# Kernel tuning notes

Measured on AMD Instinct MI355X. Metric: run time of the kernel, lower is better.

## Reference

```python
import jax, jax.numpy as jnp
import numpy as np

N_COARSE = 262145   # GMGN self.n
K_LEVELS = 5        # self.k
M_NBR = 9           # self.m
HID = 2048          # hidden_channels


def _build_grid():
    # replicates GMGN.init_toep_kernel (mtype='toep_mg')
    n_fine = 2 * (N_COARSE - 1) + 1          # 524289
    x = np.linspace(-1.0, 1.0, n_fine)
    x_lst, idx_lst = [], []
    for _ in range(K_LEVELS):
        n = x.shape[0]
        idx = np.arange((n - 1) // 2 - M_NBR + 1, (n - 1) // 2 + M_NBR)[1::2]  # m-1 center pts
        idx_lst.append(idx)
        x_lst.append(x[idx])
        x = x[::2]                            # injection1d
    x_lst.append(x)                           # coarse grid
    xs = np.concatenate(x_lst)[:, None].astype(np.float32)   # (N_eval, 1)
    nbrs = np.stack(idx_lst[::-1]).astype(np.int64)          # (k, m-1), coarse->fine
    return xs, nbrs


def setup_inputs() -> dict:
    key = jax.random.key(0)
    xs_np, nbrs_np = _build_grid()
    dims = [1, HID, HID, HID, HID, 1]
    inp = {"xs": jnp.asarray(xs_np), "nbrs": jnp.asarray(nbrs_np), "k": K_LEVELS, "m": M_NBR}
    ks = jax.random.split(key, 10)
    for j in range(5):
        bd = 1.0 / np.sqrt(dims[j])           # nn.Linear default init range
        inp[f"w{j}"] = jax.random.uniform(ks[2 * j], (dims[j], dims[j + 1]), jnp.float32, -bd, bd)
        inp[f"b{j}"] = jax.random.uniform(ks[2 * j + 1], (dims[j + 1],), jnp.float32, -bd, bd)
    return inp


def _interp1d(a):
    # linear prolongation: (n,) -> (2n-1,); even slots copy, odd slots average
    out = jnp.zeros((2 * a.shape[0] - 1,), a.dtype)
    out = out.at[0::2].set(a)
    return out.at[1::2].set(0.5 * (a[:-1] + a[1:]))


def _forward(xs, Ws, bs, nbrs, k, m):
    h = xs
    for W, b in zip(Ws, bs):
        h = jax.nn.relu(h @ W + b)            # MLP appends relu after every Linear (incl. last)
    Amg = h[:, 0]                             # (N_eval,) pointwise kernel values
    band = m - 1
    Abands = [Amg[band * i: band * (i + 1)] for i in range(k)][::-1]
    Ah = Amg[band * k:]                       # coarse kernel, length (n0-1)/2^k + 1
    for i in range(k):
        Ah = _interp1d(Ah)                    # upsample one level
        Ah = Ah.at[nbrs[i]].set(Abands[i])    # overwrite center band with exact MLP evals
    return Ah[None, None]                     # (1, 1, 2*(n-1)+1)


def reference(xs, w0, b0, w1, b1, w2, b2, w3, b3, w4, b4, nbrs, k, m):
    return _forward(xs, (w0, w1, w2, w3, w4), (b0, b1, b2, b3, b4), nbrs, k, m)
```

## Files before the change

### kernel.cpp

```cpp
#include <hip/hip_runtime.h>
#include <stdint.h>

#define HID    2048
#define MPTS   16425
#define MTILES 129
#define NTIL   16
#define KTIL   64
#define BIMG   5120

typedef float    f32x4 __attribute__((ext_vector_type(4)));
typedef _Float16 f16x8 __attribute__((ext_vector_type(8)));


__global__ void pack_w16(const float* __restrict__ w1,
                         const float* __restrict__ w2,
                         const float* __restrict__ w3,
                         _Float16* __restrict__ wp) {
    const int kt = blockIdx.x, nt = blockIdx.y, L = blockIdx.z;
    const float* W = (L == 0) ? w1 : ((L == 1) ? w2 : w3);
    __shared__ float tl[128 * 33];
    const int tid = threadIdx.x;
    const int k  = tid >> 3;
    const int nc = (tid & 7) * 16;
    const float* src = W + (size_t)(kt * 32 + k) * HID + nt * 128 + nc;
    #pragma unroll
    for (int j = 0; j < 16; ++j) tl[(nc + j) * 33 + k] = src[j];
    __syncthreads();
    const size_t base = (size_t)(L * 1024 + nt * 64 + kt) * BIMG;
    for (int e = tid; e < BIMG; e += 256) {
        int n = e / 40, kk = e - n * 40;
        wp[base + e] = (kk < 32) ? (_Float16)tl[n * 33 + kk] : (_Float16)0.f;
    }
}

__launch_bounds__(256, 3)
__global__ void gemm_hl(const _Float16* __restrict__ Ahg,
                        const _Float16* __restrict__ Alg,
                        const _Float16* __restrict__ wp,
                        const float* __restrict__ bias,
                        _Float16* __restrict__ Chg,
                        _Float16* __restrict__ Clg,
                        int layer, int write_lo,
                        float* __restrict__ Amg4,
                        const float* __restrict__ w4g, int row0) {
    __shared__ _Float16 Bs[4][BIMG];

    const int tid  = threadIdx.x;
    const int lane = tid & 63;
    const int wave = tid >> 6;
    const int quad = lane >> 4;
    const int lidx = lane & 15;

    const int nwg = (int)(gridDim.x * gridDim.y);
    const int L   = (int)(blockIdx.y * gridDim.x + blockIdx.x);
    const int F   = (L & 7) * (nwg >> 3) + (L >> 3);
    const int nt  = F & 15;
    const int mt  = F >> 4;

    const int mbase = wave * 32;

    const char* gW = (const char*)(wp + (size_t)(layer * 1024 + nt * 64) * BIMG);

    const size_t abase = ((size_t)(mt * 64) << 12) + (size_t)(mbase >> 4) * 512 + (size_t)lane * 8;
    const _Float16* aH = Ahg + abase;
    const _Float16* aL = Alg + abase;

    f32x4 acc[2][8];
    #pragma unroll
    for (int i = 0; i < 2; ++i)
        #pragma unroll
        for (int j = 0; j < 8; ++j) acc[i][j] = (f32x4)0.f;

#define PF_B(KT, BUF) do {                                                            \
    const char* nW_ = gW + (size_t)(KT) * (BIMG * 2);                                 \
    char* dW_ = (char*)&Bs[BUF][0];                                                   \
    for (int t = wave; t < 10; t += 4) {                                              \
        __builtin_amdgcn_global_load_lds(                                             \
            (const __attribute__((address_space(1))) unsigned int*)(nW_ + t * 1024 + lane * 16), \
            (__attribute__((address_space(3))) unsigned int*)(dW_ + t * 1024), 16, 0, 0); \
    }                                                                                 \
} while (0)

#define LD_A(KT, H, Lo) do {                                                          \
    const size_t ak_ = (size_t)(KT) << 12;                                            \
    _Pragma("unroll")                                                                 \
    for (int mm = 0; mm < 2; ++mm) {                                                  \
        H[mm]  = *(const f16x8*)(aH + ak_ + mm * 512);                                \
        Lo[mm] = *(const f16x8*)(aL + ak_ + mm * 512);                                \
    }                                                                                 \
} while (0)

#define LD_B(BUF, BF) do {                                                            \
    _Pragma("unroll")                                                                 \
    for (int nn = 0; nn < 8; ++nn) {                                                  \
        int r_ = nn * 16 + lidx;                                                      \
        BF[nn] = *(const f16x8*)(&Bs[BUF][r_ * 40 + quad * 8]);                       \
    }                                                                                 \
} while (0)

#define MFMA32(AH, AL, BF) do {                                                       \
    _Pragma("unroll")                                                                 \
    for (int mm = 0; mm < 2; ++mm)                                                    \
        _Pragma("unroll")                                                             \
        for (int nn = 0; nn < 8; ++nn) {                                              \
            acc[mm][nn] = __builtin_amdgcn_mfma_f32_16x16x32_f16(AH[mm], BF[nn], acc[mm][nn], 0, 0, 0); \
            acc[mm][nn] = __builtin_amdgcn_mfma_f32_16x16x32_f16(AL[mm], BF[nn], acc[mm][nn], 0, 0, 0); \
        }                                                                             \
} while (0)

#define GATE4() do {                                                                  \
    asm volatile("s_waitcnt vmcnt(4)" ::: "memory");                                  \
    __builtin_amdgcn_sched_barrier(0);                                                \
    __builtin_amdgcn_s_barrier();                                                     \
    __builtin_amdgcn_sched_barrier(0);                                                \
} while (0)

#define SUPER(S, P, DO_PF, DO_A2) do {                                                \
    f16x8 bfr0_[8];                                                                   \
    LD_B(2 * (P), bfr0_);                                                             \
    if (DO_PF) { PF_B(2 * (S) + 2, 2 * ((P) ^ 1)); PF_B(2 * (S) + 3, 2 * ((P) ^ 1) + 1); } \
    LD_A(2 * (S) + 1, nah, nal);                                                      \
    MFMA32(cah, cal, bfr0_);                                                          \
    f16x8 bfr1_[8];                                                                   \
    LD_B(2 * (P) + 1, bfr1_);                                                         \
    if (DO_A2) LD_A(2 * (S) + 2, cah, cal);                                           \
    MFMA32(nah, nal, bfr1_);                                                          \
    GATE4();                                                                          \
} while (0)

    f16x8 cah[2], cal[2], nah[2], nal[2];

    PF_B(0, 0);
    PF_B(1, 1);
    LD_A(0, cah, cal);
    __syncthreads();

    for (int ss = 0; ss < 15; ++ss) {
        SUPER(2 * ss,     0, 1, 1);
        SUPER(2 * ss + 1, 1, 1, 1);
    }
    SUPER(30, 0, 1, 1);
    SUPER(31, 1, 0, 0);

#undef SUPER
#undef GATE4
#undef MFMA32
#undef LD_B
#undef LD_A
#undef PF_B

    if (Amg4) {
        float w4v[8], bv[8];
        #pragma unroll
        for (int nn = 0; nn < 8; ++nn) {
            const int col = nt * 128 + nn * 16 + lidx;
            w4v[nn] = w4g[col];
            bv[nn]  = bias[col];
        }
        #pragma unroll
        for (int mm = 0; mm < 2; ++mm) {
            #pragma unroll
            for (int r = 0; r < 4; ++r) {
                float p = 0.f;
                #pragma unroll
                for (int nn = 0; nn < 8; ++nn) {
                    float v = acc[mm][nn][r] + bv[nn];
                    v = v > 0.f ? v : 0.f;
                    p += v * w4v[nn];
                }
                #pragma unroll
                for (int off = 1; off <= 8; off <<= 1)
                    p += __shfl_xor(p, off, 16);
                if (lidx == 0) {
                    const int grow = row0 + mt * 128 + mbase + mm * 16 + quad * 4 + r;
                    if (grow < MPTS) atomicAdd(Amg4 + grow, p);
                }
            }
        }
        return;
    }

    #pragma unroll
    for (int nn = 0; nn < 8; ++nn) {
        const int col = nt * 128 + nn * 16 + lidx;
        const float bv = bias[col];
        const int kt2 = col >> 5, quad2 = (col >> 3) & 3, j2 = col & 7;
        const size_t cb = ((size_t)(mt * 64 + kt2) << 12) + quad2 * 128 + j2;
        #pragma unroll
        for (int mm = 0; mm < 2; ++mm) {
            const int rowg = (mbase >> 4) + mm;
            #pragma unroll
            for (int r = 0; r < 4; ++r) {
                const int lidx2 = quad * 4 + r;
                float v = acc[mm][nn][r] + bv;
                v = v > 0.f ? v : 0.f;
                _Float16 hs = (_Float16)v;
                const size_t idx = cb + rowg * 512 + lidx2 * 8;
                Chg[idx] = hs;
                if (write_lo) Clg[idx] = (_Float16)(v - (float)hs);
            }
        }
    }
}

__launch_bounds__(256, 3)
__global__ void gemm_f0(const float* __restrict__ xs,
                        const float* __restrict__ w0f,
                        const float* __restrict__ b0f,
                        const _Float16* __restrict__ wp,
                        const float* __restrict__ bias,
                        _Float16* __restrict__ Chg,
                        _Float16* __restrict__ Clg, int row0) {
    __shared__ _Float16 Bs[4][BIMG];

    const int tid  = threadIdx.x;
    const int lane = tid & 63;
    const int wave = tid >> 6;
    const int quad = lane >> 4;
    const int lidx = lane & 15;

    const int nwg = (int)(gridDim.x * gridDim.y);
    const int L   = (int)(blockIdx.y * gridDim.x + blockIdx.x);
    const int F   = (L & 7) * (nwg >> 3) + (L >> 3);
    const int nt  = F & 15;
    const int mt  = F >> 4;

    const int mbase = wave * 32;

    const char* gW = (const char*)(wp + (size_t)(nt * 64) * BIMG);

    const int g0 = row0 + mt * 128 + mbase + lidx;
    const float x0 = (g0 < MPTS) ? xs[g0] : 0.f;
    const float x1 = (g0 + 16 < MPTS) ? xs[g0 + 16] : 0.f;

    f32x4 acc[2][8];
    #pragma unroll
    for (int i = 0; i < 2; ++i)
        #pragma unroll
        for (int j = 0; j < 8; ++j) acc[i][j] = (f32x4)0.f;

#define PF0(KT, BUF) do {                                                             \
    const char* nW_ = gW + (size_t)(KT) * (BIMG * 2);                                 \
    char* dW_ = (char*)&Bs[BUF][0];                                                   \
    for (int t = wave; t < 10; t += 4) {                                              \
        __builtin_amdgcn_global_load_lds(                                             \
            (const __attribute__((address_space(1))) unsigned int*)(nW_ + t * 1024 + lane * 16), \
            (__attribute__((address_space(3))) unsigned int*)(dW_ + t * 1024), 16, 0, 0); \
    }                                                                                 \
} while (0)

#define LDW0(KT, WA, WB, BA, BB) do {                                                 \
    const int k0_ = (KT) * 32 + quad * 8;                                             \
    WA = *(const f32x4*)(w0f + k0_);                                                  \
    WB = *(const f32x4*)(w0f + k0_ + 4);                                              \
    BA = *(const f32x4*)(b0f + k0_);                                                  \
    BB = *(const f32x4*)(b0f + k0_ + 4);                                              \
} while (0)

#define COMP0(WA, WB, BA, BB) do {                                                    \
    _Pragma("unroll")                                                                 \
    for (int mm = 0; mm < 2; ++mm) {                                                  \
        const float xm_ = mm ? x1 : x0;                                               \
        f16x8 h_, l_;                                                                 \
        _Pragma("unroll")                                                             \
        for (int j = 0; j < 4; ++j) {                                                 \
            float v_ = xm_ * WA[j] + BA[j];                                           \
            v_ = v_ > 0.f ? v_ : 0.f;                                                 \
            _Float16 hs_ = (_Float16)v_;                                              \
            h_[j] = hs_; l_[j] = (_Float16)(v_ - (float)hs_);                         \
        }                                                                             \
        _Pragma("unroll")                                                             \
        for (int j = 0; j < 4; ++j) {                                                 \
            float v_ = xm_ * WB[j] + BB[j];                                           \
            v_ = v_ > 0.f ? v_ : 0.f;                                                 \
            _Float16 hs_ = (_Float16)v_;                                              \
            h_[4 + j] = hs_; l_[4 + j] = (_Float16)(v_ - (float)hs_);                 \
        }                                                                             \
        cah[mm] = h_; cal[mm] = l_;                                                   \
    }                                                                                 \
} while (0)

#define LDB0(BUF, BF) do {                                                            \
    _Pragma("unroll")                                                                 \
    for (int nn = 0; nn < 8; ++nn) {                                                  \
        int r_ = nn * 16 + lidx;                                                      \
        BF[nn] = *(const f16x8*)(&Bs[BUF][r_ * 40 + quad * 8]);                       \
    }                                                                                 \
} while (0)

#define MFMA0(BF) do {                                                                \
    _Pragma("unroll")                                                                 \
    for (int mm = 0; mm < 2; ++mm)                                                    \
        _Pragma("unroll")                                                             \
        for (int nn = 0; nn < 8; ++nn) {                                              \
            acc[mm][nn] = __builtin_amdgcn_mfma_f32_16x16x32_f16(cah[mm], BF[nn], acc[mm][nn], 0, 0, 0); \
            acc[mm][nn] = __builtin_amdgcn_mfma_f32_16x16x32_f16(cal[mm], BF[nn], acc[mm][nn], 0, 0, 0); \
        }                                                                             \
} while (0)

#define GATE0() do {                                                                  \
    asm volatile("s_waitcnt vmcnt(4)" ::: "memory");                                  \
    __builtin_amdgcn_sched_barrier(0);                                                \
    __builtin_amdgcn_s_barrier();                                                     \
    __builtin_amdgcn_sched_barrier(0);                                                \
} while (0)

#define SUPERF(S, P, DO_PF, DO_W2) do {                                               \
    f16x8 bfr0_[8];                                                                   \
    LDB0(2 * (P), bfr0_);                                                             \
    if (DO_PF) { PF0(2 * (S) + 2, 2 * ((P) ^ 1)); PF0(2 * (S) + 3, 2 * ((P) ^ 1) + 1); } \
    LDW0(2 * (S) + 1, wBa, wBb, bBa, bBb);                                            \
    COMP0(wAa, wAb, bAa, bAb);                                             \
    MFMA0(bfr0_);                                                                     \
    f16x8 bfr1_[8];                                                                   \
    LDB0(2 * (P) + 1, bfr1_);                                                         \
    if (DO_W2) LDW0(2 * (S) + 2, wAa, wAb, bAa, bAb);                                 \
    COMP0(wBa, wBb, bBa, bBb);             \
    MFMA0(bfr1_);                                                                     \
    GATE0();                                 \
} while (0)

    f16x8 cah[2], cal[2];
    f32x4 wAa, wAb, bAa, bAb, wBa, wBb, bBa, bBb;

    PF0(0, 0);
    PF0(1, 1);
    LDW0(0, wAa, wAb, bAa, bAb);
    __syncthreads();

    for (int ss = 0; ss < 15; ++ss) {
        SUPERF(2 * ss,     0, 1, 1);
        SUPERF(2 * ss + 1, 1, 1, 1);
    }
    SUPERF(30, 0, 1, 1);
    SUPERF(31, 1, 0, 0);

#undef SUPERF
#undef GATE0
#undef MFMA0
#undef LDB0
#undef COMP0
#undef LDW0
#undef PF0

    #pragma unroll
    for (int nn = 0; nn < 8; ++nn) {
        const int col = nt * 128 + nn * 16 + lidx;
        const float bv = bias[col];
        const int kt2 = col >> 5, quad2 = (col >> 3) & 3, j2 = col & 7;
        const size_t cb = ((size_t)(mt * 64 + kt2) << 12) + quad2 * 128 + j2;
        #pragma unroll
        for (int mm = 0; mm < 2; ++mm) {
            const int rowg = (mbase >> 4) + mm;
            #pragma unroll
            for (int r = 0; r < 4; ++r) {
                const int lidx2 = quad * 4 + r;
                float v = acc[mm][nn][r] + bv;
                v = v > 0.f ? v : 0.f;
                _Float16 hs = (_Float16)v;
                const size_t idx = cb + rowg * 512 + lidx2 * 8;
                Chg[idx] = hs;
                Clg[idx] = (_Float16)(v - (float)hs);
            }
        }
    }
}

__global__ void layer0f(const float* __restrict__ xs, const float* __restrict__ w0,
                        const float* __restrict__ b0, float* __restrict__ A, int row0) {
    const int r = blockIdx.x;
    const int j = threadIdx.x * 8;
    const float x = (row0 + r < MPTS) ? xs[row0 + r] : 0.f;
    float* out = A + (size_t)r * HID + j;
    #pragma unroll
    for (int q = 0; q < 8; ++q) {
        float v = x * w0[j + q] + b0[j + q];
        out[q] = v > 0.f ? v : 0.f;
    }
}

__launch_bounds__(256)
__global__ void gemm_valu(const float* __restrict__ A, const float* __restrict__ W,
                          const float* __restrict__ bias, float* __restrict__ C) {
    __shared__ float As[16][132];
    __shared__ float Ws[16][132];
    const int tid = threadIdx.x;
    const int tx = tid & 15, ty = tid >> 4;
    const int n0 = blockIdx.x * 128;
    const int m0 = blockIdx.y * 128;
    const int am = tid & 127, ak = (tid >> 7) * 8;
    const int wn = (tid & 15) * 8, wk = tid >> 4;
    const float* aptr = A + (size_t)(m0 + am) * HID + ak;
    const float* wptr = W + (size_t)wk * HID + n0 + wn;
    float acc[8][8];
    #pragma unroll
    for (int i = 0; i < 8; ++i)
        #pragma unroll
        for (int j = 0; j < 8; ++j) acc[i][j] = 0.f;
    for (int k0 = 0; k0 < HID; k0 += 16) {
        f32x4 a0 = *(const f32x4*)(aptr + k0);
        f32x4 a1 = *(const f32x4*)(aptr + k0 + 4);
        f32x4 w0v = *(const f32x4*)(wptr + (size_t)k0 * HID);
        f32x4 w1v = *(const f32x4*)(wptr + (size_t)k0 * HID + 4);
        __syncthreads();
        As[ak + 0][am] = a0[0]; As[ak + 1][am] = a0[1];
        As[ak + 2][am] = a0[2]; As[ak + 3][am] = a0[3];
        As[ak + 4][am] = a1[0]; As[ak + 5][am] = a1[1];
        As[ak + 6][am] = a1[2]; As[ak + 7][am] = a1[3];
        *(f32x4*)&Ws[wk][wn]     = w0v;
        *(f32x4*)&Ws[wk][wn + 4] = w1v;
        __syncthreads();
        #pragma unroll
        for (int kk = 0; kk < 16; ++kk) {
            f32x4 av0 = *(const f32x4*)&As[kk][ty * 8];
            f32x4 av1 = *(const f32x4*)&As[kk][ty * 8 + 4];
            f32x4 bv0 = *(const f32x4*)&Ws[kk][tx * 8];
            f32x4 bv1 = *(const f32x4*)&Ws[kk][tx * 8 + 4];
            float a[8] = {av0[0], av0[1], av0[2], av0[3], av1[0], av1[1], av1[2], av1[3]};
            float b[8] = {bv0[0], bv0[1], bv0[2], bv0[3], bv1[0], bv1[1], bv1[2], bv1[3]};
            #pragma unroll
            for (int i = 0; i < 8; ++i)
                #pragma unroll
                for (int j = 0; j < 8; ++j) acc[i][j] += a[i] * b[j];
        }
    }
    #pragma unroll
    for (int i = 0; i < 8; ++i) {
        const int m = m0 + ty * 8 + i;
        #pragma unroll
        for (int jc = 0; jc < 2; ++jc) {
            const int n = n0 + tx * 8 + jc * 4;
            f32x4 v4;
            #pragma unroll
            for (int q = 0; q < 4; ++q) {
                float v = acc[i][jc * 4 + q] + bias[n + q];
                v4[q] = v > 0.f ? v : 0.f;
            }
            *(f32x4*)(C + (size_t)m * HID + n) = v4;
        }
    }
}

__global__ void layer4f(const float* __restrict__ A, const float* __restrict__ w4,
                        const float* __restrict__ b4, float* __restrict__ Amg, int row0) {
    const int lane = threadIdx.x & 63;
    const int wave = threadIdx.x >> 6;
    const int r    = blockIdx.x * 4 + wave;
    if (row0 + r >= MPTS) return;
    const float* ap = A + (size_t)r * HID;
    float s = 0.f;
    #pragma unroll
    for (int c = 0; c < 8; ++c) {
        const int col = c * 256 + lane * 4;
        f32x4 av = *(const f32x4*)(ap + col);
        f32x4 wv = *(const f32x4*)(w4 + col);
        s += av[0] * wv[0] + av[1] * wv[1] + av[2] * wv[2] + av[3] * wv[3];
    }
    #pragma unroll
    for (int off = 32; off; off >>= 1) s += __shfl_down(s, off);
    if (lane == 0) {
        float v = s + b4[0];
        Amg[row0 + r] = v > 0.f ? v : 0.f;
    }
}

__global__ void mg_level(const float* __restrict__ in, float* __restrict__ outf,
                         const int* __restrict__ nbrs_base, int level,
                         const float* __restrict__ band, int n_out,
                         const float* __restrict__ b4p, int xin) {
    const int j = blockIdx.x * 256 + threadIdx.x;
    if (j >= n_out) return;
    const float b4v = b4p ? b4p[0] : 0.f;
    float v;
    if (j & 1) {
        float a = in[j >> 1], b = in[(j >> 1) + 1];
        if (xin) { a = fmaxf(a + b4v, 0.f); b = fmaxf(b + b4v, 0.f); }
        v = 0.5f * (a + b);
    } else {
        float a = in[j >> 1];
        if (xin) a = fmaxf(a + b4v, 0.f);
        v = a;
    }
    const int stride =
        (nbrs_base[1] == 0 && nbrs_base[3] == 0 && nbrs_base[5] == 0) ? 2 : 1;
    #pragma unroll
    for (int t = 0; t < 8; ++t) {
        const int idx = nbrs_base[(level * 8 + t) * stride];
        if (j == idx) {
            float bb = band[t];
            if (b4p) bb = fmaxf(bb + b4v, 0.f);
            v = bb;
        }
    }
    outf[j] = v;
}

extern "C" void kernel_launch(void* const* d_in, const int* in_sizes, int n_in,
                              void* d_out, int out_size, void* d_ws, size_t ws_size,
                              hipStream_t stream) {
    int iXS=0, iNB=1, iW0=4, iB0=5, iW1=6, iB1=7, iW2=8, iB2=9,
        iW3=10, iB3=11, iW4=12, iB4=13;
    if (n_in >= 14) {
        if (in_sizes[0] == HID) {
            iB0=0; iB1=1; iB2=2; iB3=3; iB4=4; iNB=7;
            iW0=8; iW1=9; iW2=10; iW3=11; iW4=12; iXS=13;
        } else if (!(in_sizes[1] == 40 || in_sizes[1] == 80)) {
            iXS=0; iW0=1; iB0=2; iW1=3; iB1=4; iW2=5; iB2=6;
            iW3=7; iB3=8; iW4=9; iB4=10; iNB=11;
        }
    }
    const float* xs = (const float*)d_in[iXS];
    const int* nbrs = (const int*)d_in[iNB];
    const float* w0 = (const float*)d_in[iW0];
    const float* b0 = (const float*)d_in[iB0];
    const float* w1 = (const float*)d_in[iW1];
    const float* b1 = (const float*)d_in[iB1];
    const float* w2 = (const float*)d_in[iW2];
    const float* b2 = (const float*)d_in[iB2];
    const float* w3 = (const float*)d_in[iW3];
    const float* b3 = (const float*)d_in[iB3];
    const float* w4 = (const float*)d_in[iW4];
    const float* b4 = (const float*)d_in[iB4];

    char* ws = (char*)d_ws;
    const size_t szAmg = 66048;
    const size_t szAh1 = 524544;
    const size_t szAh2 = 1048832;
    float* Amg = (float*)(ws);
    float* ahA = (float*)(ws + szAmg);
    float* ahB = (float*)(ws + szAmg + szAh1);
    const size_t casc_end = szAmg + szAh1 + szAh2;
    const size_t szW    = (size_t)3 * 1024 * BIMG * 2;
    const size_t per_tile = 2ull * 128 * HID * 4;

    const int use_mfma = (ws_size >= casc_end + szW + per_tile) ? 1 : 0;

    _Float16* wp = (_Float16*)(ws + casc_end);
    const size_t buf_start = use_mfma ? (casc_end + szW) : casc_end;

    size_t avail = ws_size - buf_start;
    int CT = (int)(avail / per_tile);
    if (CT < 1) CT = 1;
    if (CT > MTILES) CT = MTILES;

    if (use_mfma) {
        const size_t half = (size_t)CT * 128 * HID;
        _Float16* bAh = (_Float16*)(ws + buf_start);
        _Float16* bAl = bAh + half;
        _Float16* bBh = bAh + 2 * half;
        _Float16* bBl = bAh + 3 * half;

        hipMemsetAsync(Amg, 0, (size_t)MPTS * sizeof(float), stream);

        pack_w16<<<dim3(KTIL, NTIL, 3), 256, 0, stream>>>(w1, w2, w3, wp);

        for (int t0 = 0; t0 < MTILES; t0 += CT) {
            int tiles = (MTILES - t0 < CT) ? (MTILES - t0) : CT;
            int row0 = t0 * 128;
            dim3 ggrid(NTIL, tiles);
            gemm_f0<<<ggrid, 256, 0, stream>>>(xs, w0, b0, wp, b1, bBh, bBl, row0);
            gemm_hl<<<ggrid, 256, 0, stream>>>(bBh, bBl, wp, b2, bAh, bAl, 1, 1,
                                               nullptr, nullptr, 0);
            gemm_hl<<<ggrid, 256, 0, stream>>>(bAh, bAl, wp, b3, bBh, bBl, 2, 0,
                                               Amg, w4, row0);
        }
    } else {
        float* bufA = (float*)(ws + buf_start);
        float* bufB = (float*)(ws + buf_start + (size_t)CT * 128 * HID * 4);
        for (int t0 = 0; t0 < MTILES; t0 += CT) {
            int tiles = (MTILES - t0 < CT) ? (MTILES - t0) : CT;
            int row0 = t0 * 128;
            layer0f<<<dim3(tiles * 128), 256, 0, stream>>>(xs, w0, b0, bufA, row0);
            dim3 ggrid(NTIL, tiles);
            gemm_valu<<<ggrid, 256, 0, stream>>>(bufA, w1, b1, bufB);
            gemm_valu<<<ggrid, 256, 0, stream>>>(bufB, w2, b2, bufA);
            gemm_valu<<<ggrid, 256, 0, stream>>>(bufA, w3, b3, bufB);
            layer4f<<<dim3(tiles * 32), 256, 0, stream>>>(bufB, w4, b4, Amg, row0);
        }
    }

    const float* b4p = use_mfma ? b4 : nullptr;
    const float* cur = Amg + 40;
    float* dsts[5] = {ahA, ahB, ahA, ahB, (float*)d_out};
    int n = 16385;
    for (int i = 0; i < 5; ++i) {
        int n_out = 2 * n - 1;
        mg_level<<<dim3((n_out + 255) / 256), 256, 0, stream>>>(
            cur, dsts[i], nbrs, i, Amg + 8 * (4 - i), n_out,
            b4p, (i == 0 && use_mfma) ? 1 : 0);
        cur = dsts[i];
        n = n_out;
    }
    (void)out_size;
}
```

Baseline: 893.8 us.

## Fuse five multigrid prolongation launches into one LDS-staged kernel

Replaces the five per-level mg_level launches with a single mg_all kernel. Each block computes the range of coarse points its 256 fine outputs depend on and runs the upsampling through all levels in shared memory. This removes four kernel launches and the intermediate global-memory round trips through ahA/ahB. In exchange it adds redundant coarse-level work per block and four block-wide barriers.

```diff
diff --git a/kernel.cpp b/kernel.cpp
--- a/kernel.cpp
+++ b/kernel.cpp
@@ -315,9 +315,9 @@
     f16x8 bfr1_[8];                                                                   \
     LDB0(2 * (P) + 1, bfr1_);                                                         \
     if (DO_W2) LDW0(2 * (S) + 2, wAa, wAb, bAa, bAb);                                 \
-    COMP0(wBa, wBb, bBa, bBb);             \
+    COMP0(wBa, wBb, bBa, bBb);                                           \
     MFMA0(bfr1_);                                                                     \
-    GATE0();                                 \
+    GATE0();                                                                          \
 } while (0)
 
     f16x8 cah[2], cal[2];
@@ -464,35 +464,77 @@
     }
 }
 
-__global__ void mg_level(const float* __restrict__ in, float* __restrict__ outf,
-                         const int* __restrict__ nbrs_base, int level,
-                         const float* __restrict__ band, int n_out,
-                         const float* __restrict__ b4p, int xin) {
-    const int j = blockIdx.x * 256 + threadIdx.x;
-    if (j >= n_out) return;
+__global__ void mg_all(const float* __restrict__ Amg, float* __restrict__ outf,
+                       const int* __restrict__ nbrs, const float* __restrict__ b4p) {
+    __shared__ float Lb[16], L0[24], L1[40], L2[72], L3[136];
+    const int t = threadIdx.x;
+    const int NFIN = 524289;
+    const int o0 = (int)blockIdx.x * 256;
     const float b4v = b4p ? b4p[0] : 0.f;
-    float v;
-    if (j & 1) {
-        float a = in[j >> 1], b = in[(j >> 1) + 1];
-        if (xin) { a = fmaxf(a + b4v, 0.f); b = fmaxf(b + b4v, 0.f); }
-        v = 0.5f * (a + b);
-    } else {
-        float a = in[j >> 1];
-        if (xin) a = fmaxf(a + b4v, 0.f);
-        v = a;
-    }
-    const int stride =
-        (nbrs_base[1] == 0 && nbrs_base[3] == 0 && nbrs_base[5] == 0) ? 2 : 1;
-    #pragma unroll
-    for (int t = 0; t < 8; ++t) {
-        const int idx = nbrs_base[(level * 8 + t) * stride];
-        if (j == idx) {
-            float bb = band[t];
-            if (b4p) bb = fmaxf(bb + b4v, 0.f);
-            v = bb;
-        }
-    }
-    outf[j] = v;
+    const int stride = (nbrs[1] == 0 && nbrs[3] == 0 && nbrs[5] == 0) ? 2 : 1;
+
+#define MGF(x) (b4p ? fmaxf((x) + b4v, 0.f) : (x))
+
+    const int nin[5] = {16385, 32769, 65537, 131073, 262145};
+    int OS4 = o0;
+    int OC4 = (NFIN - o0 < 256) ? (NFIN - o0) : 256;
+    int IS4 = (OS4 > 0) ? ((OS4 - 1) >> 1) : 0;
+    int IE4 = ((OS4 + OC4) >> 1) + 1; if (IE4 > nin[4]) IE4 = nin[4];
+    int OS3 = IS4, OC3 = IE4 - IS4;
+    int IS3 = (OS3 > 0) ? ((OS3 - 1) >> 1) : 0;
+    int IE3 = ((OS3 + OC3) >> 1) + 1; if (IE3 > nin[3]) IE3 = nin[3];
+    int OS2 = IS3, OC2 = IE3 - IS3;
+    int IS2 = (OS2 > 0) ? ((OS2 - 1) >> 1) : 0;
+    int IE2 = ((OS2 + OC2) >> 1) + 1; if (IE2 > nin[2]) IE2 = nin[2];
+    int OS1 = IS2, OC1 = IE2 - IS2;
+    int IS1 = (OS1 > 0) ? ((OS1 - 1) >> 1) : 0;
+    int IE1 = ((OS1 + OC1) >> 1) + 1; if (IE1 > nin[1]) IE1 = nin[1];
+    int OS0 = IS1, OC0 = IE1 - IS1;
+    int IS0 = (OS0 > 0) ? ((OS0 - 1) >> 1) : 0;
+    int IE0 = ((OS0 + OC0) >> 1) + 1; if (IE0 > nin[0]) IE0 = nin[0];
+    int BS = IS0, BC = IE0 - IS0;
+
+    if (t < BC) Lb[t] = MGF(Amg[40 + BS + t]);
+    __syncthreads();
+
+#define MG_STAGE(LVL, INARR, INS, OUTARR, OS_, OC_) do {                              \
+    if (t < (OC_)) {                                                                  \
+        const int gj = (OS_) + t;                                                     \
+        const int h = gj >> 1;                                                        \
+        float v;                                                                      \
+        if (gj & 1) v = 0.5f * (INARR[h - (INS)] + INARR[h + 1 - (INS)]);             \
+        else        v = INARR[h - (INS)];                                             \
+        _Pragma("unroll")                                                             \
+        for (int t8 = 0; t8 < 8; ++t8) {                                              \
+            const int idx = nbrs[((LVL) * 8 + t8) * stride];                          \
+            if (idx == gj) v = MGF(Amg[8 * (4 - (LVL)) + t8]);                        \
+        }                                                                             \
+        OUTARR[t] = v;                                                                \
+    }                                                                                 \
+    __syncthreads();                                                                  \
+} while (0)
+
+    MG_STAGE(0, Lb, BS,  L0, OS0, OC0);
+    MG_STAGE(1, L0, OS0, L1, OS1, OC1);
+    MG_STAGE(2, L1, OS1, L2, OS2, OC2);
+    MG_STAGE(3, L2, OS2, L3, OS3, OC3);
+
+    if (t < OC4) {
+        const int gj = OS4 + t;
+        const int h = gj >> 1;
+        float v;
+        if (gj & 1) v = 0.5f * (L3[h - OS3] + L3[h + 1 - OS3]);
+        else        v = L3[h - OS3];
+        #pragma unroll
+        for (int t8 = 0; t8 < 8; ++t8) {
+            const int idx = nbrs[(4 * 8 + t8) * stride];
+            if (idx == gj) v = MGF(Amg[t8]);
+        }
+        outf[gj] = v;
+    }
+
+#undef MG_STAGE
+#undef MGF
 }
 
 extern "C" void kernel_launch(void* const* d_in, const int* in_sizes, int n_in,
@@ -580,16 +622,8 @@
     }
 
     const float* b4p = use_mfma ? b4 : nullptr;
-    const float* cur = Amg + 40;
-    float* dsts[5] = {ahA, ahB, ahA, ahB, (float*)d_out};
-    int n = 16385;
-    for (int i = 0; i < 5; ++i) {
-        int n_out = 2 * n - 1;
-        mg_level<<<dim3((n_out + 255) / 256), 256, 0, stream>>>(
-            cur, dsts[i], nbrs, i, Amg + 8 * (4 - i), n_out,
-            b4p, (i == 0 && use_mfma) ? 1 : 0);
-        cur = dsts[i];
-        n = n_out;
-    }
+    mg_all<<<dim3((524289 + 255) / 256), 256, 0, stream>>>(
+        Amg, (float*)d_out, nbrs, b4p);
+    (void)ahA; (void)ahB;
     (void)out_size;
 }
```

Measured after the change: 876.2 us (median of 2 runs). -2.0%, faster.
